# Performance work log

Measured on AMD Instinct MI355X. Metric: run time of the kernel, lower is better.

Reference implementation:

```python
import jax, jax.numpy as jnp
import numpy as np

HID_NUM = 2  # inner-layer loop count (all iterations use layer-0 weights, as in the source)


def setup_inputs() -> dict:
    key = jax.random.key(0)
    k_x, k_emb, k_w1, k_fcw, k_fcb = jax.random.split(key, 5)
    T, B, H, V, C = 512, 64, 1024, 32000, 32000
    x = jax.random.randint(k_x, (T, B), 0, V)
    emb = jax.random.normal(k_emb, (V, H), dtype=jnp.float32)  # nn.Embedding default N(0,1)
    w1 = jax.random.normal(k_w1, (H, 6 * H), dtype=jnp.float32) * 0.014  # ~N(0,2)*0.01
    b1 = jnp.zeros((1, 6 * H), dtype=jnp.float32)
    fc_w = jax.random.normal(k_fcw, (C, H), dtype=jnp.float32) * 0.03
    fc_b = jnp.zeros((C,), dtype=jnp.float32)
    return {"x": x, "emb": emb, "w1": w1, "b1": b1, "fc_w": fc_w, "fc_b": fc_b}


def reference(x, emb, w1, b1, fc_w, fc_b):
    H = w1.shape[0]
    Wx = w1[:, :H]           # input-to-hidden
    Wh = w1[:, H:2 * H]      # hidden-to-hidden (cols 2H:6H of w1 are unused, as in source)
    b = b1[:, :H]            # only first H bias entries are used
    xe = emb[x]                                        # (T, B, H)
    xin = jnp.einsum('tbh,hk->tbk', xe, Wx) + b        # precompute input projections (T, B, H)
    # t == 0: h0 is zeros so its Wh contribution vanishes; the hid_num-fold
    # inner loop re-reads h0 every iteration, so the result is idempotent.
    h0 = jnp.tanh(xin[0])                              # (B, H)

    def step(h, xin_t):
        for _ in range(HID_NUM):                       # cell applied hid_num times per step
            h = jnp.tanh(xin_t + h @ Wh)
        return h, h

    h_last, hs = jax.lax.scan(step, h0, xin[1:])       # hs: (T-1, B, H)
    out = jnp.concatenate([h0[None], hs], axis=0)      # (T, B, H)
    B_ = out.shape[1]
    out = jnp.transpose(out, (1, 0, 2)).reshape(B_, -1)  # torch.cat(out, 1) -> (B, T*H)
    y = h_last @ fc_w.T + fc_b                         # (B, class_num)
    return (y, out)
```

## Files before the change

kernel.cpp:

```cpp
#include <hip/hip_runtime.h>
#include <hip/hip_bf16.h>

#define T_DIM 512
#define B_DIM 64
#define H_DIM 1024
#define C_DIM 32000
#define W1_LD 6144
#define TH    (T_DIM * H_DIM)

typedef __attribute__((ext_vector_type(8))) short s16x8;
typedef __attribute__((ext_vector_type(4))) float f32x4;

__device__ __forceinline__ unsigned short bf_rne(float f) {
    union { float f; unsigned u; } v; v.f = f;
    unsigned u = v.u;
    return (unsigned short)((u + 0x7FFFu + ((u >> 16) & 1u)) >> 16);
}
__device__ __forceinline__ float bf2f(unsigned short s) {
    union { unsigned u; float f; } v; v.u = ((unsigned)s) << 16;
    return v.f;
}
__device__ __forceinline__ s16x8 pack_bf(f32x4 a, f32x4 b) {
    s16x8 o;
    o[0] = (short)bf_rne(a[0]); o[1] = (short)bf_rne(a[1]);
    o[2] = (short)bf_rne(a[2]); o[3] = (short)bf_rne(a[3]);
    o[4] = (short)bf_rne(b[0]); o[5] = (short)bf_rne(b[1]);
    o[6] = (short)bf_rne(b[2]); o[7] = (short)bf_rne(b[3]);
    return o;
}

#define OFF_XIN 0
#define OFF_WXP 67108864UL
#define OFF_WHP 69206016UL
#define OFF_H   71303168UL
#define OFF_CNT 71565312UL

__global__ void pack_w(const float* __restrict__ w1,
                       unsigned short* __restrict__ wxp,
                       unsigned short* __restrict__ whp) {
    unsigned f = blockIdx.x * 256 + threadIdx.x;
    unsigned j  = f & 7u;
    unsigned l  = (f >> 3) & 63u;
    unsigned kb = (f >> 9) & 31u;
    unsigned ct = f >> 14;
    unsigned k = kb * 32u + ((l >> 4) * 8u) + j;
    unsigned c = ct * 16u + (l & 15u);
    wxp[f] = bf_rne(w1[(size_t)k * W1_LD + c]);
    whp[f] = bf_rne(w1[(size_t)k * W1_LD + 1024 + c]);
}

__global__ void gemm_xin(const int* __restrict__ x,
                         const float* __restrict__ emb,
                         const unsigned short* __restrict__ wxp,
                         const float* __restrict__ b1,
                         unsigned short* __restrict__ xin) {
    const int wave = threadIdx.x >> 6;
    const int lane = threadIdx.x & 63;
    const int quad = lane >> 4;
    const int n16  = lane & 15;
    const int id = blockIdx.x * 4 + wave;
    const int mj = id >> 4;
    const int nj = id & 15;

    int idxv[4];
    #pragma unroll
    for (int i = 0; i < 4; ++i)
        idxv[i] = x[(size_t)(mj * 64 + i * 16 + n16)];

    float bias[4];
    #pragma unroll
    for (int n = 0; n < 4; ++n)
        bias[n] = b1[nj * 64 + n * 16 + n16];

    f32x4 acc[4][4];
    #pragma unroll
    for (int i = 0; i < 4; ++i)
        #pragma unroll
        for (int n = 0; n < 4; ++n)
            acc[i][n] = (f32x4){0.f, 0.f, 0.f, 0.f};

    for (int kb = 0; kb < 32; ++kb) {
        s16x8 a[4];
        #pragma unroll
        for (int i = 0; i < 4; ++i) {
            const float* ap = emb + (size_t)idxv[i] * H_DIM + kb * 32 + quad * 8;
            f32x4 lo = *(const f32x4*)ap;
            f32x4 hi = *(const f32x4*)(ap + 4);
            a[i] = pack_bf(lo, hi);
        }
        s16x8 b[4];
        #pragma unroll
        for (int n = 0; n < 4; ++n)
            b[n] = *(const s16x8*)(wxp + (size_t)((nj * 4 + n) * 32 + kb) * 512 + lane * 8);
        #pragma unroll
        for (int i = 0; i < 4; ++i)
            #pragma unroll
            for (int n = 0; n < 4; ++n)
                acc[i][n] = __builtin_amdgcn_mfma_f32_16x16x32_bf16(a[i], b[n], acc[i][n], 0, 0, 0);
    }

    #pragma unroll
    for (int i = 0; i < 4; ++i)
        #pragma unroll
        for (int n = 0; n < 4; ++n)
            #pragma unroll
            for (int r = 0; r < 4; ++r) {
                int row = mj * 64 + i * 16 + quad * 4 + r;
                int col = nj * 64 + n * 16 + n16;
                xin[(size_t)row * H_DIM + col] = bf_rne(acc[i][n][r] + bias[n]);
            }
}

__device__ __forceinline__ void group_barrier(unsigned* cnt, unsigned target) {
    __syncthreads();
    if (threadIdx.x == 0) {
        __hip_atomic_fetch_add(cnt, 1u, __ATOMIC_RELEASE, __HIP_MEMORY_SCOPE_AGENT);
        while (__hip_atomic_load(cnt, __ATOMIC_ACQUIRE, __HIP_MEMORY_SCOPE_AGENT) < target)
            __builtin_amdgcn_s_sleep(2);
    }
    __syncthreads();
}

__global__ __launch_bounds__(256, 1) void rnn_recur(
        const unsigned short* __restrict__ xin,
        const unsigned short* __restrict__ whp,
        unsigned short* __restrict__ hbuf,
        float* __restrict__ out,
        unsigned* __restrict__ cnt) {
    const int g    = blockIdx.x;
    const int p    = g & 3;
    const int qg   = g >> 2;
    const int wave = threadIdx.x >> 6;
    const int lane = threadIdx.x & 63;
    const int quad = lane >> 4;
    const int n16  = lane & 15;
    const int ct   = qg * 4 + wave;
    const int c    = ct * 16 + n16;

    s16x8 bfr[32];
    #pragma unroll
    for (int kb = 0; kb < 32; ++kb)
        bfr[kb] = *(const s16x8*)(whp + (size_t)(ct * 32 + kb) * 512 + lane * 8);

    unsigned* myc = cnt + p * 64;
    unsigned target = 0;

    const int arow  = p * 16 + n16;
    const int orow0 = p * 16 + quad * 4;

    float xf[4], val[4];

    #pragma unroll
    for (int r = 0; r < 4; ++r)
        xf[r] = bf2f(xin[(size_t)(orow0 + r) * H_DIM + c]);
    #pragma unroll
    for (int r = 0; r < 4; ++r) {
        val[r] = tanhf(xf[r]);
        hbuf[(size_t)(orow0 + r) * H_DIM + c] = bf_rne(val[r]);
        out[(size_t)(orow0 + r) * TH + c] = val[r];
    }
    target += 16;
    group_barrier(myc, target);

    int s = 1;
    for (int t = 1; t < T_DIM; ++t) {
        #pragma unroll
        for (int r = 0; r < 4; ++r)
            xf[r] = bf2f(xin[(size_t)(t * B_DIM + orow0 + r) * H_DIM + c]);
        #pragma unroll
        for (int it = 0; it < 2; ++it) {
            const unsigned short* hr = hbuf + (size_t)((s + 1) & 1) * (B_DIM * H_DIM);
            unsigned short*       hw = hbuf + (size_t)(s & 1) * (B_DIM * H_DIM);
            const unsigned short* abase = hr + (size_t)arow * H_DIM + quad * 8;

            f32x4 acc0 = {0.f, 0.f, 0.f, 0.f};
            f32x4 acc1 = {0.f, 0.f, 0.f, 0.f};
            #pragma unroll
            for (int kb = 0; kb < 32; kb += 2) {
                s16x8 a0 = *(const s16x8*)(abase + kb * 32);
                s16x8 a1 = *(const s16x8*)(abase + kb * 32 + 32);
                acc0 = __builtin_amdgcn_mfma_f32_16x16x32_bf16(a0, bfr[kb],     acc0, 0, 0, 0);
                acc1 = __builtin_amdgcn_mfma_f32_16x16x32_bf16(a1, bfr[kb + 1], acc1, 0, 0, 0);
            }
            #pragma unroll
            for (int r = 0; r < 4; ++r) {
                val[r] = tanhf(xf[r] + acc0[r] + acc1[r]);
                hw[(size_t)(orow0 + r) * H_DIM + c] = bf_rne(val[r]);
            }
            if (it == 1) {
                #pragma unroll
                for (int r = 0; r < 4; ++r)
                    out[(size_t)(orow0 + r) * TH + (size_t)t * H_DIM + c] = val[r];
            }
            target += 16;
            group_barrier(myc, target);
            ++s;
        }
    }
}

__global__ void gemm_y(const unsigned short* __restrict__ hlast,
                       const float* __restrict__ fc_w,
                       const float* __restrict__ fc_b,
                       float* __restrict__ y) {
    const int wave = threadIdx.x >> 6;
    const int lane = threadIdx.x & 63;
    const int quad = lane >> 4;
    const int n16  = lane & 15;
    const int id = blockIdx.x * 4 + wave;
    const int n0 = id * 16;

    f32x4 acc[4];
    #pragma unroll
    for (int i = 0; i < 4; ++i) acc[i] = (f32x4){0.f, 0.f, 0.f, 0.f};

    for (int kb = 0; kb < 32; ++kb) {
        const float* bp = fc_w + (size_t)(n0 + n16) * H_DIM + kb * 32 + quad * 8;
        s16x8 b = pack_bf(*(const f32x4*)bp, *(const f32x4*)(bp + 4));
        #pragma unroll
        for (int i = 0; i < 4; ++i) {
            s16x8 a = *(const s16x8*)(hlast + (size_t)(i * 16 + n16) * H_DIM + kb * 32 + quad * 8);
            acc[i] = __builtin_amdgcn_mfma_f32_16x16x32_bf16(a, b, acc[i], 0, 0, 0);
        }
    }

    const int cc = n0 + n16;
    const float bias = fc_b[cc];
    #pragma unroll
    for (int i = 0; i < 4; ++i)
        #pragma unroll
        for (int r = 0; r < 4; ++r)
            y[(size_t)(i * 16 + quad * 4 + r) * C_DIM + cc] = acc[i][r] + bias;
}

extern "C" void kernel_launch(void* const* d_in, const int* in_sizes, int n_in,
                              void* d_out, int out_size, void* d_ws, size_t ws_size,
                              hipStream_t stream) {
    const int*   x    = (const int*)  d_in[0];
    const float* emb  = (const float*)d_in[1];
    const float* w1   = (const float*)d_in[2];
    const float* b1   = (const float*)d_in[3];
    const float* fc_w = (const float*)d_in[4];
    const float* fc_b = (const float*)d_in[5];

    char* ws = (char*)d_ws;
    unsigned short* xin  = (unsigned short*)(ws + OFF_XIN);
    unsigned short* wxp  = (unsigned short*)(ws + OFF_WXP);
    unsigned short* whp  = (unsigned short*)(ws + OFF_WHP);
    unsigned short* hbuf = (unsigned short*)(ws + OFF_H);
    unsigned*       cnt  = (unsigned*)(ws + OFF_CNT);

    float* y    = (float*)d_out;
    float* outp = (float*)d_out + (size_t)B_DIM * C_DIM;

    hipMemsetAsync(ws + OFF_CNT, 0, 1024, stream);
    pack_w  <<<4096, 256, 0, stream>>>(w1, wxp, whp);
    gemm_xin<<<2048, 256, 0, stream>>>(x, emb, wxp, b1, xin);
    rnn_recur<<<64,  256, 0, stream>>>(xin, whp, hbuf, outp, cnt);
    gemm_y  <<<500,  256, 0, stream>>>(hbuf, fc_w, fc_b, y);
}
```

Measured before the change: 7.594 ms.

## Store hidden history in-place in xin buffer and expand to fp32 output afterward

The recurrent kernel now overwrites each timestep's xin slice with the bf16 hidden state and uses a single temp buffer for the intermediate inner iteration. This removes the strided fp32 output stores from the latency-bound serial loop. A separate fully parallel kernel then converts the bf16 history into the transposed fp32 output. The barrier spin now uses relaxed loads plus one acquire fence and a shorter sleep. In exchange, the output is rounded to bf16 precision and an extra pass over the data is added.

```diff
diff --git a/kernel.cpp b/kernel.cpp
--- a/kernel.cpp
+++ b/kernel.cpp
@@ -10,6 +10,7 @@
 
 typedef __attribute__((ext_vector_type(8))) short s16x8;
 typedef __attribute__((ext_vector_type(4))) float f32x4;
+typedef __attribute__((ext_vector_type(4))) unsigned short u16x4;
 
 __device__ __forceinline__ unsigned short bf_rne(float f) {
     union { float f; unsigned u; } v; v.f = f;
@@ -32,7 +33,7 @@
 #define OFF_XIN 0
 #define OFF_WXP 67108864UL
 #define OFF_WHP 69206016UL
-#define OFF_H   71303168UL
+#define OFF_HT  71303168UL
 #define OFF_CNT 71565312UL
 
 __global__ void pack_w(const float* __restrict__ w1,
@@ -115,17 +116,17 @@
     __syncthreads();
     if (threadIdx.x == 0) {
         __hip_atomic_fetch_add(cnt, 1u, __ATOMIC_RELEASE, __HIP_MEMORY_SCOPE_AGENT);
-        while (__hip_atomic_load(cnt, __ATOMIC_ACQUIRE, __HIP_MEMORY_SCOPE_AGENT) < target)
-            __builtin_amdgcn_s_sleep(2);
+        while (__hip_atomic_load(cnt, __ATOMIC_RELAXED, __HIP_MEMORY_SCOPE_AGENT) < target)
+            __builtin_amdgcn_s_sleep(1);
+        __builtin_amdgcn_fence(__ATOMIC_ACQUIRE, "agent");
     }
     __syncthreads();
 }
 
 __global__ __launch_bounds__(256, 1) void rnn_recur(
-        const unsigned short* __restrict__ xin,
+        unsigned short* __restrict__ hist,
         const unsigned short* __restrict__ whp,
-        unsigned short* __restrict__ hbuf,
-        float* __restrict__ out,
+        unsigned short* __restrict__ htmp,
         unsigned* __restrict__ cnt) {
     const int g    = blockIdx.x;
     const int p    = g & 3;
@@ -152,25 +153,23 @@
 
     #pragma unroll
     for (int r = 0; r < 4; ++r)
-        xf[r] = bf2f(xin[(size_t)(orow0 + r) * H_DIM + c]);
-    #pragma unroll
-    for (int r = 0; r < 4; ++r) {
-        val[r] = tanhf(xf[r]);
-        hbuf[(size_t)(orow0 + r) * H_DIM + c] = bf_rne(val[r]);
-        out[(size_t)(orow0 + r) * TH + c] = val[r];
-    }
+        xf[r] = bf2f(hist[(size_t)(orow0 + r) * H_DIM + c]);
+    #pragma unroll
+    for (int r = 0; r < 4; ++r)
+        hist[(size_t)(orow0 + r) * H_DIM + c] = bf_rne(tanhf(xf[r]));
     target += 16;
     group_barrier(myc, target);
 
-    int s = 1;
     for (int t = 1; t < T_DIM; ++t) {
+        unsigned short* xt = hist + (size_t)t * (B_DIM * H_DIM);
         #pragma unroll
         for (int r = 0; r < 4; ++r)
-            xf[r] = bf2f(xin[(size_t)(t * B_DIM + orow0 + r) * H_DIM + c]);
+            xf[r] = bf2f(xt[(size_t)(orow0 + r) * H_DIM + c]);
         #pragma unroll
         for (int it = 0; it < 2; ++it) {
-            const unsigned short* hr = hbuf + (size_t)((s + 1) & 1) * (B_DIM * H_DIM);
-            unsigned short*       hw = hbuf + (size_t)(s & 1) * (B_DIM * H_DIM);
+            const unsigned short* hr = (it == 0)
+                ? hist + (size_t)(t - 1) * (B_DIM * H_DIM) : htmp;
+            unsigned short* hw = (it == 0) ? htmp : xt;
             const unsigned short* abase = hr + (size_t)arow * H_DIM + quad * 8;
 
             f32x4 acc0 = {0.f, 0.f, 0.f, 0.f};
@@ -187,16 +186,22 @@
                 val[r] = tanhf(xf[r] + acc0[r] + acc1[r]);
                 hw[(size_t)(orow0 + r) * H_DIM + c] = bf_rne(val[r]);
             }
-            if (it == 1) {
-                #pragma unroll
-                for (int r = 0; r < 4; ++r)
-                    out[(size_t)(orow0 + r) * TH + (size_t)t * H_DIM + c] = val[r];
-            }
             target += 16;
             group_barrier(myc, target);
-            ++s;
         }
     }
+}
+
+__global__ void hist_to_out(const unsigned short* __restrict__ hist,
+                            float* __restrict__ out) {
+    size_t i = ((size_t)blockIdx.x * 256 + threadIdx.x) * 4;
+    unsigned h = (unsigned)(i & 1023u);
+    unsigned b = (unsigned)((i >> 10) & 63u);
+    unsigned t = (unsigned)(i >> 16);
+    u16x4 v = *(const u16x4*)(hist + i);
+    f32x4 o;
+    o[0] = bf2f(v[0]); o[1] = bf2f(v[1]); o[2] = bf2f(v[2]); o[3] = bf2f(v[3]);
+    *(f32x4*)(out + (size_t)b * TH + (size_t)t * H_DIM + h) = o;
 }
 
 __global__ void gemm_y(const unsigned short* __restrict__ hlast,
@@ -247,15 +252,17 @@
     unsigned short* xin  = (unsigned short*)(ws + OFF_XIN);
     unsigned short* wxp  = (unsigned short*)(ws + OFF_WXP);
     unsigned short* whp  = (unsigned short*)(ws + OFF_WHP);
-    unsigned short* hbuf = (unsigned short*)(ws + OFF_H);
+    unsigned short* htmp = (unsigned short*)(ws + OFF_HT);
     unsigned*       cnt  = (unsigned*)(ws + OFF_CNT);
 
     float* y    = (float*)d_out;
     float* outp = (float*)d_out + (size_t)B_DIM * C_DIM;
 
     hipMemsetAsync(ws + OFF_CNT, 0, 1024, stream);
-    pack_w  <<<4096, 256, 0, stream>>>(w1, wxp, whp);
-    gemm_xin<<<2048, 256, 0, stream>>>(x, emb, wxp, b1, xin);
-    rnn_recur<<<64,  256, 0, stream>>>(xin, whp, hbuf, outp, cnt);
-    gemm_y  <<<500,  256, 0, stream>>>(hbuf, fc_w, fc_b, y);
-}
+    pack_w     <<<4096, 256, 0, stream>>>(w1, wxp, whp);
+    gemm_xin   <<<2048, 256, 0, stream>>>(x, emb, wxp, b1, xin);
+    rnn_recur  <<<64,   256, 0, stream>>>(xin, whp, htmp, cnt);
+    hist_to_out<<<32768, 256, 0, stream>>>(xin, outp);
+    gemm_y     <<<500,  256, 0, stream>>>(xin + (size_t)(T_DIM - 1) * B_DIM * H_DIM,
+                                          fc_w, fc_b, y);
+}
```

New measurement: 6.781 ms. 10.7% less time.
